# Kernel tuning notes

Hardware: AMD Instinct MI355X
Metric: run time of the kernel (lower is better)

## Reference

```python
import jax, jax.numpy as jnp
import numpy as np

LATENT = 256
MID = 512
T = 5          # num_transforms
OUT = T * 6 + T  # 35
THRESH = 0.9   # MATRIX_NORM_THRESHOLD
EPS = 1e-5     # torch LayerNorm eps
B = 131072


def _xavier(key, fan_in, fan_out):
    lim = np.sqrt(6.0 / (fan_in + fan_out)).astype(np.float32)
    return jax.random.uniform(key, (fan_in, fan_out), jnp.float32, -lim, lim)


def setup_inputs() -> dict:
    key = jax.random.key(0)
    ks = jax.random.split(key, 8)
    z = jax.random.normal(ks[0], (B, LATENT), jnp.float32)
    W1 = _xavier(ks[1], LATENT, MID)
    Wa = _xavier(ks[2], MID, MID)
    Wb = _xavier(ks[3], MID, MID)
    Wout = _xavier(ks[4], MID, OUT)
    bias = lambda n: jnp.full((n,), 0.01, jnp.float32)  # nn.init.constant_(bias, 0.01)
    return {
        "z": z,
        "W1": W1, "b1": bias(MID), "g1": jnp.ones((MID,), jnp.float32), "be1": jnp.zeros((MID,), jnp.float32),
        "Wa": Wa, "ba": bias(MID), "ga": jnp.ones((MID,), jnp.float32), "bea": jnp.zeros((MID,), jnp.float32),
        "Wb": Wb, "bb": bias(MID), "gb": jnp.ones((MID,), jnp.float32), "beb": jnp.zeros((MID,), jnp.float32),
        "Wout": Wout, "bout": bias(OUT),
    }


def _layernorm(x, g, b):
    mu = jnp.mean(x, axis=-1, keepdims=True)
    var = jnp.mean(jnp.square(x - mu), axis=-1, keepdims=True)
    return (x - mu) * jax.lax.rsqrt(var + EPS) * g + b


def reference(z, W1, b1, g1, be1, Wa, ba, ga, bea, Wb, bb, gb, beb, Wout, bout):
    # Linear -> LayerNorm -> ReLU
    h = jax.nn.relu(_layernorm(z @ W1 + b1, g1, be1))
    # ResidualBlock: Linear -> LN -> SiLU -> Linear -> LN, then skip add
    y = jax.nn.silu(_layernorm(h @ Wa + ba, ga, bea))
    y = _layernorm(y @ Wb + bb, gb, beb)
    h = h + y
    x = h @ Wout + bout                     # [B, 35]

    affines = x[:, : T * 6].reshape(-1, T, 2, 3)  # [B, T, 2, 3]
    logits = x[:, T * 6:]                         # [B, T]
    probs = jax.nn.softmax(logits, axis=-1)

    M = affines[..., :2]                          # [B, T, 2, 2]
    U, S, Vh = jnp.linalg.svd(M, full_matrices=False)
    Sc = jnp.minimum(S, THRESH)                   # clamp(max=0.9)
    M2 = jnp.einsum("btij,btj,btjk->btik", U, Sc, Vh)
    affines = jnp.concatenate([M2, affines[..., 2:]], axis=-1)
    return affines, probs
```

## Files before the change

### kernel.cpp

```cpp
#include <hip/hip_runtime.h>
#include <hip/hip_bf16.h>

#define BQ     131072
#define NLAT   256
#define NMID   512
#define NT     5
#define NOUT   35
#define NOUTP  48

typedef unsigned short u16;
typedef unsigned int   u32;
typedef unsigned long long u64;
typedef __attribute__((ext_vector_type(8))) short bf16x8;
typedef __attribute__((ext_vector_type(4))) float f32x4;

__device__ __forceinline__ u16 f2bf(float x) {
  union { float f; u32 u; } v; v.f = x;
  u32 r = (v.u + 0x7FFFu + ((v.u >> 16) & 1u)) >> 16;
  return (u16)r;
}

__global__ __launch_bounds__(256) void transpose_cast(
    const float* __restrict__ src, u16* __restrict__ dst, int K, int N, int NP) {
  __shared__ float tile[32][33];
  int kx = blockIdx.x * 32, ny = blockIdx.y * 32;
  int tx = threadIdx.x, ty = threadIdx.y;
#pragma unroll
  for (int i = 0; i < 4; i++) {
    int k = kx + ty + i * 8, n = ny + tx;
    tile[ty + i * 8][tx] = (k < K && n < N) ? src[(size_t)k * N + n] : 0.f;
  }
  __syncthreads();
#pragma unroll
  for (int i = 0; i < 4; i++) {
    int n = ny + ty + i * 8, k = kx + tx;
    if (n < NP && k < K) dst[(size_t)n * K + k] = f2bf(tile[tx][ty + i * 8]);
  }
}

template <int K, int ACT>
__device__ __forceinline__ void layer(
    const u16* __restrict__ wt, const float* __restrict__ bias,
    const float* __restrict__ gam, const float* __restrict__ bet,
    const u16* src, u16* dst,
    float (*sStat)[64][2], float (*sFin)[2],
    int tid, int wid, int l15, int lg, int wfb)
{
  f32x4 acc[4][4];
#pragma unroll
  for (int m = 0; m < 4; m++)
#pragma unroll
    for (int n = 0; n < 4; n++) acc[m][n] = (f32x4){0.f, 0.f, 0.f, 0.f};

  for (int kb = 0; kb < K; kb += 32) {
    int k0 = kb + lg * 8;
    bf16x8 a[4], bf[4];
#pragma unroll
    for (int m = 0; m < 4; m++)
      a[m] = *(const bf16x8*)(wt + (size_t)(wfb + m * 16 + l15) * K + k0);
#pragma unroll
    for (int n = 0; n < 4; n++) {
      int b = n * 16 + l15;
      int byte = (b * (K * 2) + k0 * 2) ^ ((b & 7) << 4);
      bf[n] = *(const bf16x8*)((const char*)src + byte);
    }
#pragma unroll
    for (int m = 0; m < 4; m++)
#pragma unroll
      for (int n = 0; n < 4; n++)
        acc[m][n] = __builtin_amdgcn_mfma_f32_16x16x32_bf16(a[m], bf[n], acc[m][n], 0, 0, 0);
  }

#pragma unroll
  for (int m = 0; m < 4; m++) {
    f32x4 bv = *(const f32x4*)(bias + wfb + m * 16 + lg * 4);
#pragma unroll
    for (int n = 0; n < 4; n++)
#pragma unroll
      for (int r = 0; r < 4; r++) acc[m][n][r] += bv[r];
  }

  float s[4], q[4];
#pragma unroll
  for (int n = 0; n < 4; n++) {
    s[n] = 0.f; q[n] = 0.f;
#pragma unroll
    for (int m = 0; m < 4; m++)
#pragma unroll
      for (int r = 0; r < 4; r++) { float v = acc[m][n][r]; s[n] += v; q[n] += v * v; }
    s[n] += __shfl_xor(s[n], 16); q[n] += __shfl_xor(q[n], 16);
    s[n] += __shfl_xor(s[n], 32); q[n] += __shfl_xor(q[n], 32);
  }
  if (lg == 0) {
#pragma unroll
    for (int n = 0; n < 4; n++) {
      int b = n * 16 + l15;
      sStat[wid][b][0] = s[n]; sStat[wid][b][1] = q[n];
    }
  }
  __syncthreads();
  if (tid < 64) {
    float ss = 0.f, qq = 0.f;
#pragma unroll
    for (int w = 0; w < 8; w++) { ss += sStat[w][tid][0]; qq += sStat[w][tid][1]; }
    float mean = ss * (1.f / 512.f);
    float var  = qq * (1.f / 512.f) - mean * mean;
    sFin[tid][0] = mean;
    sFin[tid][1] = rsqrtf(var + 1e-5f);
  }
  __syncthreads();

  float mean[4], rstd[4];
#pragma unroll
  for (int n = 0; n < 4; n++) {
    int b = n * 16 + l15;
    mean[n] = sFin[b][0]; rstd[n] = sFin[b][1];
  }
#pragma unroll
  for (int m = 0; m < 4; m++) {
    int f0 = wfb + m * 16 + lg * 4;
    f32x4 gv  = *(const f32x4*)(gam + f0);
    f32x4 bev = *(const f32x4*)(bet + f0);
#pragma unroll
    for (int n = 0; n < 4; n++) {
      int b = n * 16 + l15;
      u16 pk[4];
#pragma unroll
      for (int r = 0; r < 4; r++) {
        float v = (acc[m][n][r] - mean[n]) * rstd[n] * gv[r] + bev[r];
        if (ACT == 1) v = fmaxf(v, 0.f);
        else if (ACT == 2) v = v / (1.f + __expf(-v));
        pk[r] = f2bf(v);
      }
      u64 w64 = (u64)pk[0] | ((u64)pk[1] << 16) | ((u64)pk[2] << 32) | ((u64)pk[3] << 48);
      int byte = (b * 1024 + f0 * 2) ^ ((b & 7) << 4);
      *(u64*)((char*)dst + byte) = w64;
    }
  }
  __syncthreads();
}

__global__ __launch_bounds__(512, 1) void ifs_main(
    const float* __restrict__ z,
    const u16* __restrict__ wt1, const u16* __restrict__ wta,
    const u16* __restrict__ wtb, const u16* __restrict__ wtout,
    const float* __restrict__ b1, const float* __restrict__ g1, const float* __restrict__ be1,
    const float* __restrict__ ba, const float* __restrict__ ga, const float* __restrict__ bea,
    const float* __restrict__ bb, const float* __restrict__ gb, const float* __restrict__ beb,
    const float* __restrict__ bout, float* __restrict__ out)
{
  __shared__ u16   sA[64 * 512];
  __shared__ u16   sB[64 * 512];
  __shared__ float sX[64 * 48];
  __shared__ float sStat[8][64][2];
  __shared__ float sFin[64][2];

  const int tid  = threadIdx.x;
  const int lane = tid & 63, wid = tid >> 6;
  const int l15  = lane & 15, lg = lane >> 4;
  const int bbase = blockIdx.x * 64;
  const int wfb   = wid * 64;

#pragma unroll
  for (int i = 0; i < 8; i++) {
    int c = tid + i * 512;
    int b = c >> 6, kc = c & 63;
    const float4 v = *(const float4*)(z + (size_t)(bbase + b) * 256 + kc * 4);
    u32 lo = (u32)f2bf(v.x) | ((u32)f2bf(v.y) << 16);
    u32 hi = (u32)f2bf(v.z) | ((u32)f2bf(v.w) << 16);
    u64 pk = (u64)lo | ((u64)hi << 32);
    int byte = (b * 512 + kc * 8) ^ ((b & 7) << 4);
    *(u64*)((char*)sB + byte) = pk;
  }
  __syncthreads();

  layer<256, 1>(wt1, b1, g1, be1, sB, sA, sStat, sFin, tid, wid, l15, lg, wfb);
  layer<512, 2>(wta, ba, ga, bea, sA, sB, sStat, sFin, tid, wid, l15, lg, wfb);
  layer<512, 0>(wtb, bb, gb, beb, sB, sB, sStat, sFin, tid, wid, l15, lg, wfb);

  {
    const int nf = wid & 3, kh = wid >> 2;
    f32x4 xacc[3];
#pragma unroll
    for (int m = 0; m < 3; m++) xacc[m] = (f32x4){0.f, 0.f, 0.f, 0.f};
    const int b = nf * 16 + l15;
    for (int kb = kh * 256; kb < kh * 256 + 256; kb += 32) {
      int k0 = kb + lg * 8;
      int byte = (b * 1024 + k0 * 2) ^ ((b & 7) << 4);
      bf16x8 bh = *(const bf16x8*)((const char*)sA + byte);
      bf16x8 by = *(const bf16x8*)((const char*)sB + byte);
#pragma unroll
      for (int m = 0; m < 3; m++) {
        bf16x8 aw = *(const bf16x8*)(wtout + (size_t)(m * 16 + l15) * 512 + k0);
        xacc[m] = __builtin_amdgcn_mfma_f32_16x16x32_bf16(aw, bh, xacc[m], 0, 0, 0);
        xacc[m] = __builtin_amdgcn_mfma_f32_16x16x32_bf16(aw, by, xacc[m], 0, 0, 0);
      }
    }
    if (kh == 0) {
#pragma unroll
      for (int m = 0; m < 3; m++)
        *(f32x4*)&sX[b * 48 + m * 16 + lg * 4] = xacc[m];
    }
    __syncthreads();
    if (kh == 1) {
#pragma unroll
      for (int m = 0; m < 3; m++) {
        f32x4* p = (f32x4*)&sX[b * 48 + m * 16 + lg * 4];
        f32x4 t = *p;
#pragma unroll
        for (int r = 0; r < 4; r++) t[r] += xacc[m][r];
        *p = t;
      }
    }
    __syncthreads();
  }

  if (tid < 64) {
    int b = tid;
    float l[5], mx = -1e30f;
#pragma unroll
    for (int j = 0; j < 5; j++) { l[j] = sX[b * 48 + 30 + j] + bout[30 + j]; mx = fmaxf(mx, l[j]); }
    float ssum = 0.f, e[5];
#pragma unroll
    for (int j = 0; j < 5; j++) { e[j] = __expf(l[j] - mx); ssum += e[j]; }
    float inv = 1.f / ssum;
    float* op = out + (size_t)BQ * 30 + (size_t)(bbase + b) * 5;
#pragma unroll
    for (int j = 0; j < 5; j++) op[j] = e[j] * inv;
  }
  for (int idx = tid; idx < 64 * NT; idx += 512) {
    int b = idx / 5, t = idx - b * 5;
    const float* xr = &sX[b * 48 + t * 6];
    float a   = xr[0] + bout[t * 6 + 0];
    float bb_ = xr[1] + bout[t * 6 + 1];
    float tx  = xr[2] + bout[t * 6 + 2];
    float c   = xr[3] + bout[t * 6 + 3];
    float d   = xr[4] + bout[t * 6 + 4];
    float ty  = xr[5] + bout[t * 6 + 5];
    float E = 0.5f * (a + d), F = 0.5f * (a - d);
    float G = 0.5f * (c + bb_), H = 0.5f * (c - bb_);
    float Q = sqrtf(E * E + H * H), R = sqrtf(F * F + G * G);
    float sx = Q + R, sy = Q - R;
    float a1 = atan2f(G, F), a2 = atan2f(H, E);
    float th = 0.5f * (a2 - a1), ph = 0.5f * (a2 + a1);
    float sxc = fminf(sx, 0.9f);
    float syc = fminf(fmaxf(sy, -0.9f), 0.9f);
    float st, ct, sp, cp;
    __sincosf(th, &st, &ct);
    __sincosf(ph, &sp, &cp);
    float ux = cp * sxc, uy = sp * sxc, vx = sp * syc, vy = cp * syc;
    float m00 =  ux * ct - vx * st;
    float m01 = -ux * st - vx * ct;
    float m10 =  uy * ct + vy * st;
    float m11 = -uy * st + vy * ct;
    float* op = out + (size_t)(bbase + b) * 30 + t * 6;
    op[0] = m00; op[1] = m01; op[2] = tx;
    op[3] = m10; op[4] = m11; op[5] = ty;
  }
}

extern "C" void kernel_launch(void* const* d_in, const int* in_sizes, int n_in,
                              void* d_out, int out_size, void* d_ws, size_t ws_size,
                              hipStream_t stream) {
  const float* z    = (const float*)d_in[0];
  const float* W1   = (const float*)d_in[1];
  const float* b1   = (const float*)d_in[2];
  const float* g1   = (const float*)d_in[3];
  const float* be1  = (const float*)d_in[4];
  const float* Wa   = (const float*)d_in[5];
  const float* ba   = (const float*)d_in[6];
  const float* ga   = (const float*)d_in[7];
  const float* bea  = (const float*)d_in[8];
  const float* Wb   = (const float*)d_in[9];
  const float* bb   = (const float*)d_in[10];
  const float* gb   = (const float*)d_in[11];
  const float* beb  = (const float*)d_in[12];
  const float* Wout = (const float*)d_in[13];
  const float* bout = (const float*)d_in[14];
  float* out = (float*)d_out;

  char* w = (char*)d_ws;
  u16* wt1   = (u16*)(w);
  u16* wta   = (u16*)(w + 262144);
  u16* wtb   = (u16*)(w + 786432);
  u16* wtout = (u16*)(w + 1310720);

  dim3 tb(32, 8);
  transpose_cast<<<dim3(8, 16),  tb, 0, stream>>>(W1,   wt1,   256, 512, 512);
  transpose_cast<<<dim3(16, 16), tb, 0, stream>>>(Wa,   wta,   512, 512, 512);
  transpose_cast<<<dim3(16, 16), tb, 0, stream>>>(Wb,   wtb,   512, 512, 512);
  transpose_cast<<<dim3(16, 2),  tb, 0, stream>>>(Wout, wtout, 512, 35,  48);

  ifs_main<<<BQ / 64, 512, 0, stream>>>(
      z, wt1, wta, wtb, wtout,
      b1, g1, be1, ba, ga, bea, bb, gb, beb, bout, out);
}
```

Before: 664.3 us.

## Double block to 1024 threads, halve per-wave tile, single-sync LayerNorm stats

The fused MLP kernel now uses 16 waves per 64-row block, with each wave owning 32 output features instead of 64. This halves the accumulators per wave and doubles latency hiding. LayerNorm statistics are reduced by every wave reading a swizzled stats buffer and broadcasting with shuffles, which removes one barrier per layer. The K loops are fully unrolled with raised MFMA priority, and the output GEMM splits K four ways with a shared-memory reduction. Weight fragments are now reloaded from global memory by twice as many waves per block, and launch_bounds(1024,4) with about 136KB of LDS may be unrealistic.

```diff
diff --git a/kernel.cpp b/kernel.cpp
--- a/kernel.cpp
+++ b/kernel.cpp
@@ -2,17 +2,14 @@
 #include <hip/hip_bf16.h>
 
 #define BQ     131072
-#define NLAT   256
-#define NMID   512
 #define NT     5
-#define NOUT   35
-#define NOUTP  48
 
 typedef unsigned short u16;
 typedef unsigned int   u32;
 typedef unsigned long long u64;
 typedef __attribute__((ext_vector_type(8))) short bf16x8;
 typedef __attribute__((ext_vector_type(4))) float f32x4;
+typedef __attribute__((ext_vector_type(2))) float f32x2;
 
 __device__ __forceinline__ u16 f2bf(float x) {
   union { float f; u32 u; } v; v.f = x;
@@ -42,42 +39,45 @@
 __device__ __forceinline__ void layer(
     const u16* __restrict__ wt, const float* __restrict__ bias,
     const float* __restrict__ gam, const float* __restrict__ bet,
-    const u16* src, u16* dst,
-    float (*sStat)[64][2], float (*sFin)[2],
-    int tid, int wid, int l15, int lg, int wfb)
+    const u16* src, u16* dst, float* sStat,
+    int lane, int wid, int l15, int lg, int wfb)
 {
-  f32x4 acc[4][4];
-#pragma unroll
-  for (int m = 0; m < 4; m++)
+  f32x4 acc[2][4];
+#pragma unroll
+  for (int m = 0; m < 2; m++)
 #pragma unroll
     for (int n = 0; n < 4; n++) acc[m][n] = (f32x4){0.f, 0.f, 0.f, 0.f};
 
+#pragma unroll
   for (int kb = 0; kb < K; kb += 32) {
-    int k0 = kb + lg * 8;
-    bf16x8 a[4], bf[4];
-#pragma unroll
-    for (int m = 0; m < 4; m++)
+    const int k0 = kb + lg * 8;
+    bf16x8 a[2];
+#pragma unroll
+    for (int m = 0; m < 2; m++)
       a[m] = *(const bf16x8*)(wt + (size_t)(wfb + m * 16 + l15) * K + k0);
+    bf16x8 bv[4];
 #pragma unroll
     for (int n = 0; n < 4; n++) {
       int b = n * 16 + l15;
       int byte = (b * (K * 2) + k0 * 2) ^ ((b & 7) << 4);
-      bf[n] = *(const bf16x8*)((const char*)src + byte);
-    }
-#pragma unroll
-    for (int m = 0; m < 4; m++)
+      bv[n] = *(const bf16x8*)((const char*)src + byte);
+    }
+    __builtin_amdgcn_s_setprio(1);
+#pragma unroll
+    for (int m = 0; m < 2; m++)
 #pragma unroll
       for (int n = 0; n < 4; n++)
-        acc[m][n] = __builtin_amdgcn_mfma_f32_16x16x32_bf16(a[m], bf[n], acc[m][n], 0, 0, 0);
-  }
-
-#pragma unroll
-  for (int m = 0; m < 4; m++) {
-    f32x4 bv = *(const f32x4*)(bias + wfb + m * 16 + lg * 4);
+        acc[m][n] = __builtin_amdgcn_mfma_f32_16x16x32_bf16(a[m], bv[n], acc[m][n], 0, 0, 0);
+    __builtin_amdgcn_s_setprio(0);
+  }
+
+#pragma unroll
+  for (int m = 0; m < 2; m++) {
+    f32x4 bv4 = *(const f32x4*)(bias + wfb + m * 16 + lg * 4);
 #pragma unroll
     for (int n = 0; n < 4; n++)
 #pragma unroll
-      for (int r = 0; r < 4; r++) acc[m][n][r] += bv[r];
+      for (int r = 0; r < 4; r++) acc[m][n][r] += bv4[r];
   }
 
   float s[4], q[4];
@@ -85,7 +85,7 @@
   for (int n = 0; n < 4; n++) {
     s[n] = 0.f; q[n] = 0.f;
 #pragma unroll
-    for (int m = 0; m < 4; m++)
+    for (int m = 0; m < 2; m++)
 #pragma unroll
       for (int r = 0; r < 4; r++) { float v = acc[m][n][r]; s[n] += v; q[n] += v * v; }
     s[n] += __shfl_xor(s[n], 16); q[n] += __shfl_xor(q[n], 16);
@@ -95,29 +95,31 @@
 #pragma unroll
     for (int n = 0; n < 4; n++) {
       int b = n * 16 + l15;
-      sStat[wid][b][0] = s[n]; sStat[wid][b][1] = q[n];
+      int byte = b * 128 + ((wid * 8) ^ ((b & 7) << 4));
+      *(f32x2*)((char*)sStat + byte) = (f32x2){s[n], q[n]};
     }
   }
   __syncthreads();
-  if (tid < 64) {
-    float ss = 0.f, qq = 0.f;
-#pragma unroll
-    for (int w = 0; w < 8; w++) { ss += sStat[w][tid][0]; qq += sStat[w][tid][1]; }
-    float mean = ss * (1.f / 512.f);
-    float var  = qq * (1.f / 512.f) - mean * mean;
-    sFin[tid][0] = mean;
-    sFin[tid][1] = rsqrtf(var + 1e-5f);
-  }
-  __syncthreads();
+
+  float ss = 0.f, qq = 0.f;
+#pragma unroll
+  for (int j = 0; j < 8; j++) {
+    int byte = lane * 128 + ((j * 16) ^ ((lane & 7) << 4));
+    f32x4 v = *(const f32x4*)((const char*)sStat + byte);
+    ss += v[0] + v[2]; qq += v[1] + v[3];
+  }
+  float meanb = ss * (1.f / 512.f);
+  float rstdb = rsqrtf(qq * (1.f / 512.f) - meanb * meanb + 1e-5f);
 
   float mean[4], rstd[4];
 #pragma unroll
   for (int n = 0; n < 4; n++) {
-    int b = n * 16 + l15;
-    mean[n] = sFin[b][0]; rstd[n] = sFin[b][1];
-  }
-#pragma unroll
-  for (int m = 0; m < 4; m++) {
+    mean[n] = __shfl(meanb, n * 16 + l15);
+    rstd[n] = __shfl(rstdb, n * 16 + l15);
+  }
+
+#pragma unroll
+  for (int m = 0; m < 2; m++) {
     int f0 = wfb + m * 16 + lg * 4;
     f32x4 gv  = *(const f32x4*)(gam + f0);
     f32x4 bev = *(const f32x4*)(bet + f0);
@@ -140,7 +142,7 @@
   __syncthreads();
 }
 
-__global__ __launch_bounds__(512, 1) void ifs_main(
+__global__ __launch_bounds__(1024, 4) void ifs_main(
     const float* __restrict__ z,
     const u16* __restrict__ wt1, const u16* __restrict__ wta,
     const u16* __restrict__ wtb, const u16* __restrict__ wtout,
@@ -149,21 +151,20 @@
     const float* __restrict__ bb, const float* __restrict__ gb, const float* __restrict__ beb,
     const float* __restrict__ bout, float* __restrict__ out)
 {
-  __shared__ u16   sA[64 * 512];
-  __shared__ u16   sB[64 * 512];
-  __shared__ float sX[64 * 48];
-  __shared__ float sStat[8][64][2];
-  __shared__ float sFin[64][2];
+  __shared__ __align__(16) char smem[65536 * 2 + 8192];
+  u16*   sA    = (u16*)smem;
+  u16*   sB    = (u16*)(smem + 65536);
+  float* sStat = (float*)(smem + 131072);
 
   const int tid  = threadIdx.x;
   const int lane = tid & 63, wid = tid >> 6;
   const int l15  = lane & 15, lg = lane >> 4;
   const int bbase = blockIdx.x * 64;
-  const int wfb   = wid * 64;
-
-#pragma unroll
-  for (int i = 0; i < 8; i++) {
-    int c = tid + i * 512;
+  const int wfb   = wid * 32;
+
+#pragma unroll
+  for (int i = 0; i < 4; i++) {
+    int c = tid + i * 1024;
     int b = c >> 6, kc = c & 63;
     const float4 v = *(const float4*)(z + (size_t)(bbase + b) * 256 + kc * 4);
     u32 lo = (u32)f2bf(v.x) | ((u32)f2bf(v.y) << 16);
@@ -174,18 +175,19 @@
   }
   __syncthreads();
 
-  layer<256, 1>(wt1, b1, g1, be1, sB, sA, sStat, sFin, tid, wid, l15, lg, wfb);
-  layer<512, 2>(wta, ba, ga, bea, sA, sB, sStat, sFin, tid, wid, l15, lg, wfb);
-  layer<512, 0>(wtb, bb, gb, beb, sB, sB, sStat, sFin, tid, wid, l15, lg, wfb);
+  layer<256, 1>(wt1, b1, g1, be1, sB, sA, sStat, lane, wid, l15, lg, wfb);
+  layer<512, 2>(wta, ba, ga, bea, sA, sB, sStat, lane, wid, l15, lg, wfb);
+  layer<512, 0>(wtb, bb, gb, beb, sB, sB, sStat, lane, wid, l15, lg, wfb);
 
   {
     const int nf = wid & 3, kh = wid >> 2;
+    const int b  = nf * 16 + l15;
     f32x4 xacc[3];
 #pragma unroll
     for (int m = 0; m < 3; m++) xacc[m] = (f32x4){0.f, 0.f, 0.f, 0.f};
-    const int b = nf * 16 + l15;
-    for (int kb = kh * 256; kb < kh * 256 + 256; kb += 32) {
-      int k0 = kb + lg * 8;
+#pragma unroll
+    for (int kk = 0; kk < 128; kk += 32) {
+      int k0 = kh * 128 + kk + lg * 8;
       int byte = (b * 1024 + k0 * 2) ^ ((b & 7) << 4);
       bf16x8 bh = *(const bf16x8*)((const char*)sA + byte);
       bf16x8 by = *(const bf16x8*)((const char*)sB + byte);
@@ -196,66 +198,67 @@
         xacc[m] = __builtin_amdgcn_mfma_f32_16x16x32_bf16(aw, by, xacc[m], 0, 0, 0);
       }
     }
-    if (kh == 0) {
-#pragma unroll
-      for (int m = 0; m < 3; m++)
-        *(f32x4*)&sX[b * 48 + m * 16 + lg * 4] = xacc[m];
-    }
     __syncthreads();
-    if (kh == 1) {
-#pragma unroll
-      for (int m = 0; m < 3; m++) {
-        f32x4* p = (f32x4*)&sX[b * 48 + m * 16 + lg * 4];
-        f32x4 t = *p;
-#pragma unroll
-        for (int r = 0; r < 4; r++) t[r] += xacc[m][r];
-        *p = t;
-      }
-    }
+    float* sP = (float*)sA;
+#pragma unroll
+    for (int m = 0; m < 3; m++)
+      *(f32x4*)(sP + (size_t)(kh * 64 + b) * 48 + m * 16 + lg * 4) = xacc[m];
     __syncthreads();
-  }
-
-  if (tid < 64) {
-    int b = tid;
-    float l[5], mx = -1e30f;
-#pragma unroll
-    for (int j = 0; j < 5; j++) { l[j] = sX[b * 48 + 30 + j] + bout[30 + j]; mx = fmaxf(mx, l[j]); }
-    float ssum = 0.f, e[5];
-#pragma unroll
-    for (int j = 0; j < 5; j++) { e[j] = __expf(l[j] - mx); ssum += e[j]; }
-    float inv = 1.f / ssum;
-    float* op = out + (size_t)BQ * 30 + (size_t)(bbase + b) * 5;
-#pragma unroll
-    for (int j = 0; j < 5; j++) op[j] = e[j] * inv;
-  }
-  for (int idx = tid; idx < 64 * NT; idx += 512) {
-    int b = idx / 5, t = idx - b * 5;
-    const float* xr = &sX[b * 48 + t * 6];
-    float a   = xr[0] + bout[t * 6 + 0];
-    float bb_ = xr[1] + bout[t * 6 + 1];
-    float tx  = xr[2] + bout[t * 6 + 2];
-    float c   = xr[3] + bout[t * 6 + 3];
-    float d   = xr[4] + bout[t * 6 + 4];
-    float ty  = xr[5] + bout[t * 6 + 5];
-    float E = 0.5f * (a + d), F = 0.5f * (a - d);
-    float G = 0.5f * (c + bb_), H = 0.5f * (c - bb_);
-    float Q = sqrtf(E * E + H * H), R = sqrtf(F * F + G * G);
-    float sx = Q + R, sy = Q - R;
-    float a1 = atan2f(G, F), a2 = atan2f(H, E);
-    float th = 0.5f * (a2 - a1), ph = 0.5f * (a2 + a1);
-    float sxc = fminf(sx, 0.9f);
-    float syc = fminf(fmaxf(sy, -0.9f), 0.9f);
-    float st, ct, sp, cp;
-    __sincosf(th, &st, &ct);
-    __sincosf(ph, &sp, &cp);
-    float ux = cp * sxc, uy = sp * sxc, vx = sp * syc, vy = cp * syc;
-    float m00 =  ux * ct - vx * st;
-    float m01 = -ux * st - vx * ct;
-    float m10 =  uy * ct + vy * st;
-    float m11 = -uy * st + vy * ct;
-    float* op = out + (size_t)(bbase + b) * 30 + t * 6;
-    op[0] = m00; op[1] = m01; op[2] = tx;
-    op[3] = m10; op[4] = m11; op[5] = ty;
+    float* sX = (float*)sB;
+    if (tid < 768) {
+      int b2 = tid / 12, j = (tid - b2 * 12) * 4;
+      f32x4 v0 = *(const f32x4*)(sP + (size_t)(0 * 64 + b2) * 48 + j);
+      f32x4 v1 = *(const f32x4*)(sP + (size_t)(1 * 64 + b2) * 48 + j);
+      f32x4 v2 = *(const f32x4*)(sP + (size_t)(2 * 64 + b2) * 48 + j);
+      f32x4 v3 = *(const f32x4*)(sP + (size_t)(3 * 64 + b2) * 48 + j);
+#pragma unroll
+      for (int r = 0; r < 4; r++) v0[r] += v1[r] + v2[r] + v3[r];
+      *(f32x4*)(sX + (size_t)b2 * 48 + j) = v0;
+    }
+    __syncthreads();
+
+    if (tid < 64) {
+      int bb2 = tid;
+      float l[5], mx = -1e30f;
+#pragma unroll
+      for (int j = 0; j < 5; j++) { l[j] = sX[bb2 * 48 + 30 + j] + bout[30 + j]; mx = fmaxf(mx, l[j]); }
+      float ssum = 0.f, e[5];
+#pragma unroll
+      for (int j = 0; j < 5; j++) { e[j] = __expf(l[j] - mx); ssum += e[j]; }
+      float inv = 1.f / ssum;
+      float* op = out + (size_t)BQ * 30 + (size_t)(bbase + bb2) * 5;
+#pragma unroll
+      for (int j = 0; j < 5; j++) op[j] = e[j] * inv;
+    }
+    if (tid < 320) {
+      int b2 = tid / 5, t = tid - b2 * 5;
+      const float* xr = sX + b2 * 48 + t * 6;
+      float a   = xr[0] + bout[t * 6 + 0];
+      float bb_ = xr[1] + bout[t * 6 + 1];
+      float tx  = xr[2] + bout[t * 6 + 2];
+      float c   = xr[3] + bout[t * 6 + 3];
+      float d   = xr[4] + bout[t * 6 + 4];
+      float ty  = xr[5] + bout[t * 6 + 5];
+      float E = 0.5f * (a + d), F = 0.5f * (a - d);
+      float G = 0.5f * (c + bb_), H = 0.5f * (c - bb_);
+      float Q = sqrtf(E * E + H * H), R = sqrtf(F * F + G * G);
+      float sx = Q + R, sy = Q - R;
+      float a1 = atan2f(G, F), a2 = atan2f(H, E);
+      float th = 0.5f * (a2 - a1), ph = 0.5f * (a2 + a1);
+      float sxc = fminf(sx, 0.9f);
+      float syc = fminf(fmaxf(sy, -0.9f), 0.9f);
+      float st, ct, sp, cp;
+      __sincosf(th, &st, &ct);
+      __sincosf(ph, &sp, &cp);
+      float ux = cp * sxc, uy = sp * sxc, vx = sp * syc, vy = cp * syc;
+      float m00 =  ux * ct - vx * st;
+      float m01 = -ux * st - vx * ct;
+      float m10 =  uy * ct + vy * st;
+      float m11 = -uy * st + vy * ct;
+      float* op = out + (size_t)(bbase + b2) * 30 + t * 6;
+      op[0] = m00; op[1] = m01; op[2] = tx;
+      op[3] = m10; op[4] = m11; op[5] = ty;
+    }
   }
 }
 
@@ -291,7 +294,7 @@
   transpose_cast<<<dim3(16, 16), tb, 0, stream>>>(Wb,   wtb,   512, 512, 512);
   transpose_cast<<<dim3(16, 2),  tb, 0, stream>>>(Wout, wtout, 512, 35,  48);
 
-  ifs_main<<<BQ / 64, 512, 0, stream>>>(
+  ifs_main<<<BQ / 64, 1024, 0, stream>>>(
       z, wt1, wta, wtb, wtout,
       b1, g1, be1, ba, ga, bea, bb, gb, beb, bout, out);
 }
```

After: 695.7 us. +4.7%, slower.
